# Performance work log

Measured on AMD Instinct MI355X. Metric: run time of the kernel, lower is better.

Reference implementation:

```python
import jax, jax.numpy as jnp
import numpy as np

N_NODES = 50000
N_EDGES = 400000
EMB_DIM = 256
N_LAYERS = 5
MAX_NODES = 50          # nodes per graph (equal-size graphs)
N_GRAPHS = N_NODES // MAX_NODES
BN_EPS = 1e-5


def setup_inputs() -> dict:
    key = jax.random.key(0)
    ks = jax.random.split(key, 12)
    D = EMB_DIM
    x = jax.random.normal(ks[0], (N_NODES, D), dtype=jnp.float32)
    edge_index = jax.random.randint(ks[1], (2, N_EDGES), 0, N_NODES, dtype=jnp.int64)
    edge_attr = jax.random.randint(ks[2], (N_EDGES, 2), 0, 3, dtype=jnp.int64)
    batch = (jnp.arange(N_NODES, dtype=jnp.int64) // MAX_NODES)
    # per-layer parameters, stacked on leading layer axis
    s1 = 1.0 / np.sqrt(D)
    s2 = 1.0 / np.sqrt(2 * D)
    W1 = jax.random.uniform(ks[3], (N_LAYERS, D, 2 * D), jnp.float32, -s1, s1)
    b1 = jax.random.uniform(ks[4], (N_LAYERS, 2 * D), jnp.float32, -s1, s1)
    W2 = jax.random.uniform(ks[5], (N_LAYERS, 2 * D, D), jnp.float32, -s2, s2)
    b2 = jax.random.uniform(ks[6], (N_LAYERS, D), jnp.float32, -s2, s2)
    # xavier_uniform for edge embeddings
    g1 = np.sqrt(6.0 / (6 + D))
    g2 = np.sqrt(6.0 / (3 + D))
    E1 = jax.random.uniform(ks[7], (N_LAYERS, 6, D), jnp.float32, -g1, g1)
    E2 = jax.random.uniform(ks[8], (N_LAYERS, 3, D), jnp.float32, -g2, g2)
    gamma = jnp.ones((N_LAYERS, D), jnp.float32)
    beta = jnp.zeros((N_LAYERS, D), jnp.float32)
    return {"x": x, "edge_index": edge_index, "edge_attr": edge_attr,
            "batch": batch, "W1": W1, "b1": b1, "W2": W2, "b2": b2,
            "E1": E1, "E2": E2, "gamma": gamma, "beta": beta}


def reference(x, edge_index, edge_attr, batch, W1, b1, W2, b2, E1, E2, gamma, beta):
    N, D = x.shape
    # add self loops once (edge_index/edge_attr are identical every layer);
    # self-loop edge_attr fill_value = 0
    loop = jnp.arange(N, dtype=edge_index.dtype)
    src = jnp.concatenate([edge_index[0], loop])
    dst = jnp.concatenate([edge_index[1], loop])
    ea0 = jnp.concatenate([edge_attr[:, 0], jnp.zeros((N,), edge_attr.dtype)])
    ea1 = jnp.concatenate([edge_attr[:, 1], jnp.zeros((N,), edge_attr.dtype)])

    h = x
    L = W1.shape[0]
    for l in range(L):
        # GINConv: message = x_j + edge_embedding, aggr='add', update = MLP
        eemb = E1[l][ea0] + E2[l][ea1]                       # [E+N, D]
        msg = h[src] + eemb                                   # gather + add
        agg = jax.ops.segment_sum(msg, dst, num_segments=N)   # scatter-add
        h = jnp.maximum(agg @ W1[l] + b1[l], 0.0) @ W2[l] + b2[l]
        # BatchNorm1d (training mode: batch statistics over nodes)
        mu = h.mean(axis=0)
        var = h.var(axis=0)
        h = (h - mu) / jnp.sqrt(var + BN_EPS) * gamma[l] + beta[l]
        if l < L - 1:
            h = jnp.maximum(h, 0.0)  # relu (dropout p=0 is identity)

    # pad_sequence over graphs: scatter node reps into [G, MAX_NODES, D]
    G = N // MAX_NODES
    ones = jnp.ones((N,), jnp.int32)
    counts = jax.ops.segment_sum(ones, batch, num_segments=G)
    starts = jnp.cumsum(counts) - counts
    pos = jnp.arange(N) - starts[batch]
    padded = jnp.zeros((G, MAX_NODES, D), h.dtype).at[batch, pos].set(h)
    return padded
```

## Files before the change

kernel.cpp:

```cpp
#include <hip/hip_runtime.h>

#define NN 50000
#define NE 400000
#define DIM 256
#define HID 512
#define NL 5
#define BN_EPS 1e-5f
#define NB_SCAN 196

typedef float float4v __attribute__((ext_vector_type(4)));
typedef _Float16 half8 __attribute__((ext_vector_type(8)));
typedef _Float16 half4v __attribute__((ext_vector_type(4)));

__device__ __forceinline__ void gl_lds16(const void* g, void* l) {
    __builtin_amdgcn_global_load_lds((__attribute__((address_space(1))) void*)g,
                                     (__attribute__((address_space(3))) void*)l, 16, 0, 0);
}


__global__ void k_zero(int* p, int n) {
    int i = blockIdx.x * blockDim.x + threadIdx.x;
    if (i < n) p[i] = 0;
}

__global__ void k_x2h(const float* __restrict__ x, _Float16* __restrict__ xh) {
    int i = blockIdx.x * blockDim.x + threadIdx.x;
    if (i >= NN * DIM / 4) return;
    float4 v = ((const float4*)x)[i];
    half4v o;
    o.x = (_Float16)v.x; o.y = (_Float16)v.y; o.z = (_Float16)v.z; o.w = (_Float16)v.w;
    ((half4v*)xh)[i] = o;
}

__global__ void k_ctab(const float* __restrict__ E1, const float* __restrict__ E2,
                       float* __restrict__ C) {
    int b = blockIdx.x;
    int l = b / 9, ab = b % 9;
    int a = ab / 3, bb = ab % 3;
    int c = threadIdx.x;
    C[(size_t)b * DIM + c] = E1[(size_t)(l * 6 + a) * DIM + c] + E2[(size_t)(l * 3 + bb) * DIM + c];
}

__global__ void k_hist(const int* __restrict__ ei, int* __restrict__ counts) {
    int e = blockIdx.x * blockDim.x + threadIdx.x;
    if (e < NE) atomicAdd(&counts[ei[NE + e]], 1);
}

__global__ void k_bsum(const int* __restrict__ counts, int* __restrict__ bsum) {
    __shared__ int s[256];
    int t = threadIdx.x;
    int i = blockIdx.x * 256 + t;
    s[t] = (i < NN) ? counts[i] : 0;
    __syncthreads();
    for (int off = 128; off > 0; off >>= 1) {
        if (t < off) s[t] += s[t + off];
        __syncthreads();
    }
    if (t == 0) bsum[blockIdx.x] = s[0];
}

__global__ void k_bscan(const int* __restrict__ bsum, int* __restrict__ bofs) {
    __shared__ int s[256];
    int t = threadIdx.x;
    int v = (t < NB_SCAN) ? bsum[t] : 0;
    s[t] = v;
    __syncthreads();
    for (int off = 1; off < 256; off <<= 1) {
        int u = (t >= off) ? s[t - off] : 0;
        __syncthreads();
        s[t] += u;
        __syncthreads();
    }
    if (t < NB_SCAN) bofs[t] = s[t] - v;
}

__global__ void k_scatterptr(const int* __restrict__ counts, const int* __restrict__ bofs,
                             int* __restrict__ row_ptr, int* __restrict__ cursor) {
    __shared__ int s[256];
    int t = threadIdx.x;
    int i = blockIdx.x * 256 + t;
    int v = (i < NN) ? counts[i] : 0;
    s[t] = v;
    __syncthreads();
    for (int off = 1; off < 256; off <<= 1) {
        int u = (t >= off) ? s[t - off] : 0;
        __syncthreads();
        s[t] += u;
        __syncthreads();
    }
    if (i < NN) {
        int ex = bofs[blockIdx.x] + s[t] - v;
        row_ptr[i] = ex;
        cursor[i] = ex;
    }
    if (i == NN - 1) row_ptr[NN] = NE;
}

__global__ void k_fill(const int* __restrict__ ei, const int* __restrict__ ea,
                       int* __restrict__ cursor, int* __restrict__ recs) {
    int e = blockIdx.x * blockDim.x + threadIdx.x;
    if (e >= NE) return;
    int src = ei[e];
    int dst = ei[NE + e];
    int a = ea[2 * e];
    int b = ea[2 * e + 1];
    int rec = src | ((a * 3 + b) << 20);
    int pos = atomicAdd(&cursor[dst], 1);
    recs[pos] = rec;
}

__global__ void k_wt(const float* __restrict__ W, _Float16* __restrict__ T, int K, int N) {
    __shared__ float t[32][33];
    int l = blockIdx.z;
    int k0 = blockIdx.y * 32, n0 = blockIdx.x * 32;
    int tx = threadIdx.x, ty = threadIdx.y;
    const float* Wl = W + (size_t)l * K * N;
    _Float16* Tl = T + (size_t)l * N * K;
    for (int d = 0; d < 32; d += 8)
        t[ty + d][tx] = Wl[(size_t)(k0 + ty + d) * N + n0 + tx];
    __syncthreads();
    for (int d = 0; d < 32; d += 8)
        Tl[(size_t)(n0 + ty + d) * K + k0 + tx] = (_Float16)t[tx][ty + d];
}

template <bool APPLY>
__global__ __launch_bounds__(256) void k_agg(const _Float16* __restrict__ rows,
                                             const float* __restrict__ ss,
                                             const float* __restrict__ Cl,
                                             const int* __restrict__ row_ptr,
                                             const int* __restrict__ recs,
                                             _Float16* __restrict__ aggh) {
    int node = (blockIdx.x * blockDim.x + threadIdx.x) >> 6;
    int lane = threadIdx.x & 63;
    if (node >= NN) return;
    int c = lane * 4;
    float s0 = 1.f, s1 = 1.f, s2 = 1.f, s3 = 1.f, t0 = 0.f, t1 = 0.f, t2 = 0.f, t3 = 0.f;
    if (APPLY) {
        s0 = ss[c]; s1 = ss[c + 1]; s2 = ss[c + 2]; s3 = ss[c + 3];
        t0 = ss[DIM + c]; t1 = ss[DIM + c + 1]; t2 = ss[DIM + c + 2]; t3 = ss[DIM + c + 3];
    }
    float4 cv0 = *(const float4*)(Cl + c);
    half4v sv = *(const half4v*)(rows + (size_t)node * DIM + c);
    float ax, ay, az, aw;
    if (APPLY) {
        ax = fmaxf((float)sv.x * s0 + t0, 0.f) + cv0.x;
        ay = fmaxf((float)sv.y * s1 + t1, 0.f) + cv0.y;
        az = fmaxf((float)sv.z * s2 + t2, 0.f) + cv0.z;
        aw = fmaxf((float)sv.w * s3 + t3, 0.f) + cv0.w;
    } else {
        ax = (float)sv.x + cv0.x;
        ay = (float)sv.y + cv0.y;
        az = (float)sv.z + cv0.z;
        aw = (float)sv.w + cv0.w;
    }
    int e0 = row_ptr[node], e1 = row_ptr[node + 1];
    for (int e = e0; e < e1; ++e) {
        int rec = recs[e];
        int src = rec & 0xFFFFF;
        int attr = rec >> 20;
        half4v hv = *(const half4v*)(rows + (size_t)src * DIM + c);
        float4 cv = *(const float4*)(Cl + (size_t)attr * DIM + c);
        if (APPLY) {
            ax += fmaxf((float)hv.x * s0 + t0, 0.f) + cv.x;
            ay += fmaxf((float)hv.y * s1 + t1, 0.f) + cv.y;
            az += fmaxf((float)hv.z * s2 + t2, 0.f) + cv.z;
            aw += fmaxf((float)hv.w * s3 + t3, 0.f) + cv.w;
        } else {
            ax += (float)hv.x + cv.x;
            ay += (float)hv.y + cv.y;
            az += (float)hv.z + cv.z;
            aw += (float)hv.w + cv.w;
        }
    }
    half4v o;
    o.x = (_Float16)ax; o.y = (_Float16)ay; o.z = (_Float16)az; o.w = (_Float16)aw;
    *(half4v*)(aggh + (size_t)node * DIM + c) = o;
}

__global__ __launch_bounds__(256, 2) void k_mlp(const _Float16* __restrict__ A,
                                                const _Float16* __restrict__ W1t,
                                                const float* __restrict__ b1,
                                                const _Float16* __restrict__ W2t,
                                                const float* __restrict__ b2,
                                                _Float16* __restrict__ Z,
                                                float* __restrict__ stats, int M) {
    __shared__ _Float16 ldsA[64 * 128];
    __shared__ _Float16 ldsH[64 * 512];
    int tid = threadIdx.x;
    int w = tid >> 6, lane = tid & 63;
    int lm = lane & 15, lg = lane >> 4;
    int row0 = blockIdx.x * 64;

    float4v acc1[4][8];
    const float4v zero = {0.f, 0.f, 0.f, 0.f};
#pragma unroll
    for (int i = 0; i < 4; ++i)
#pragma unroll
        for (int j = 0; j < 8; ++j) acc1[i][j] = zero;

#pragma unroll
    for (int kc = 0; kc < 2; ++kc) {
        {
            int srow = lane >> 4;
            int slot = lane & 15;
#pragma unroll
            for (int j = 0; j < 4; ++j) {
                int cr = w * 16 + j * 4 + srow;
                int gr = min(row0 + cr, M - 1);
                int gk = kc * 128 + ((slot ^ (cr & 7)) * 8);
                gl_lds16(A + (size_t)gr * DIM + gk, ldsA + (w * 16 + j * 4) * 128);
            }
        }
        __syncthreads();
#pragma unroll
        for (int qq = 0; qq < 4; ++qq) {
            half8 bf[8];
#pragma unroll
            for (int nt = 0; nt < 8; ++nt) {
                int n = w * 128 + nt * 16 + lm;
                bf[nt] = *(const half8*)(W1t + (size_t)n * DIM + kc * 128 + qq * 32 + lg * 8);
            }
            half8 af[4];
#pragma unroll
            for (int mt = 0; mt < 4; ++mt) {
                int m = mt * 16 + lm;
                int slot = qq * 4 + lg;
                af[mt] = *(const half8*)(ldsA + m * 128 + ((slot ^ (m & 7)) * 8));
            }
#pragma unroll
            for (int mt = 0; mt < 4; ++mt)
#pragma unroll
                for (int nt = 0; nt < 8; ++nt)
                    acc1[mt][nt] = __builtin_amdgcn_mfma_f32_16x16x32_f16(af[mt], bf[nt],
                                                                          acc1[mt][nt], 0, 0, 0);
        }
        __syncthreads();
    }

#pragma unroll
    for (int nt = 0; nt < 8; ++nt) {
        int col = w * 128 + nt * 16 + lm;
        float bv = b1[col];
        int cs = col >> 3, ci = col & 7;
#pragma unroll
        for (int mt = 0; mt < 4; ++mt)
#pragma unroll
            for (int r = 0; r < 4; ++r) {
                int row = mt * 16 + lg * 4 + r;
                float v = fmaxf(acc1[mt][nt][r] + bv, 0.f);
                ldsH[row * 512 + ((cs ^ (row & 7)) << 3) + ci] = (_Float16)v;
            }
    }
    __syncthreads();

    float4v acc2[4][4];
#pragma unroll
    for (int i = 0; i < 4; ++i)
#pragma unroll
        for (int j = 0; j < 4; ++j) acc2[i][j] = zero;

#pragma unroll
    for (int q = 0; q < 16; ++q) {
        half8 bf[4];
#pragma unroll
        for (int nt = 0; nt < 4; ++nt) {
            int n = w * 64 + nt * 16 + lm;
            bf[nt] = *(const half8*)(W2t + (size_t)n * HID + q * 32 + lg * 8);
        }
        half8 af[4];
#pragma unroll
        for (int mt = 0; mt < 4; ++mt) {
            int m = mt * 16 + lm;
            int slot = q * 4 + lg;
            af[mt] = *(const half8*)(ldsH + m * 512 + ((slot ^ (m & 7)) << 3));
        }
#pragma unroll
        for (int mt = 0; mt < 4; ++mt)
#pragma unroll
            for (int nt = 0; nt < 4; ++nt)
                acc2[mt][nt] = __builtin_amdgcn_mfma_f32_16x16x32_f16(af[mt], bf[nt],
                                                                      acc2[mt][nt], 0, 0, 0);
    }
    __syncthreads();

    _Float16* ldsZ = ldsH;
    float psum[4], psq[4];
#pragma unroll
    for (int nt = 0; nt < 4; ++nt) { psum[nt] = 0.f; psq[nt] = 0.f; }
#pragma unroll
    for (int nt = 0; nt < 4; ++nt) {
        int col = w * 64 + nt * 16 + lm;
        float bv = b2[col];
        int cs = col >> 3, ci = col & 7;
#pragma unroll
        for (int mt = 0; mt < 4; ++mt)
#pragma unroll
            for (int r = 0; r < 4; ++r) {
                int row = mt * 16 + lg * 4 + r;
                float v = acc2[mt][nt][r] + bv;
                if (row0 + row < M) {
                    psum[nt] += v;
                    psq[nt] += v * v;
                }
                ldsZ[row * 256 + ((cs ^ (row & 7)) << 3) + ci] = (_Float16)v;
            }
    }
#pragma unroll
    for (int nt = 0; nt < 4; ++nt) {
        psum[nt] += __shfl_xor(psum[nt], 16);
        psum[nt] += __shfl_xor(psum[nt], 32);
        psq[nt] += __shfl_xor(psq[nt], 16);
        psq[nt] += __shfl_xor(psq[nt], 32);
    }
    if (lg == 0) {
#pragma unroll
        for (int nt = 0; nt < 4; ++nt) {
            int ch = w * 64 + nt * 16 + lm;
            atomicAdd(&stats[ch], psum[nt]);
            atomicAdd(&stats[DIM + ch], psq[nt]);
        }
    }
    __syncthreads();
#pragma unroll
    for (int i = 0; i < 8; ++i) {
        int s = i * 256 + tid;
        int row = s >> 5, c16 = s & 31;
        if (row0 + row < M) {
            half8 v = *(const half8*)(ldsZ + row * 256 + ((c16 ^ (row & 7)) << 3));
            *(half8*)(Z + (size_t)(row0 + row) * DIM + c16 * 8) = v;
        }
    }
}

__global__ void k_bnfin(float* __restrict__ stats, const float* __restrict__ gamma,
                        const float* __restrict__ beta, float* __restrict__ ss) {
    int c = threadIdx.x;
    float mu = stats[c] * (1.0f / NN);
    float var = stats[DIM + c] * (1.0f / NN) - mu * mu;
    float sc = gamma[c] / sqrtf(var + BN_EPS);
    ss[c] = sc;
    ss[DIM + c] = beta[c] - mu * sc;
    stats[c] = 0.f;
    stats[DIM + c] = 0.f;
}

__global__ void k_out(const _Float16* __restrict__ z, const float* __restrict__ ss,
                      float* __restrict__ out) {
    int i = blockIdx.x * blockDim.x + threadIdx.x;
    if (i >= NN * DIM / 4) return;
    int c4 = (i & (DIM / 4 - 1)) * 4;
    half4v v = ((const half4v*)z)[i];
    float4 o;
    o.x = (float)v.x * ss[c4] + ss[DIM + c4];
    o.y = (float)v.y * ss[c4 + 1] + ss[DIM + c4 + 1];
    o.z = (float)v.z * ss[c4 + 2] + ss[DIM + c4 + 2];
    o.w = (float)v.w * ss[c4 + 3] + ss[DIM + c4 + 3];
    ((float4*)out)[i] = o;
}

extern "C" void kernel_launch(void* const* d_in, const int* in_sizes, int n_in,
                              void* d_out, int out_size, void* d_ws, size_t ws_size,
                              hipStream_t stream) {
    const float* x = (const float*)d_in[0];
    const int* ei = (const int*)d_in[1];
    const int* ea = (const int*)d_in[2];
    const float* W1 = (const float*)d_in[4];
    const float* b1 = (const float*)d_in[5];
    const float* W2 = (const float*)d_in[6];
    const float* b2 = (const float*)d_in[7];
    const float* E1 = (const float*)d_in[8];
    const float* E2 = (const float*)d_in[9];
    const float* gamma = (const float*)d_in[10];
    const float* beta = (const float*)d_in[11];
    float* out = (float*)d_out;

    char* w = (char*)d_ws;
    _Float16* xh = (_Float16*)w;   w += (size_t)NN * DIM * 2;
    _Float16* z = (_Float16*)w;    w += (size_t)NN * DIM * 2;
    _Float16* aggh = (_Float16*)w; w += (size_t)NN * DIM * 2;
    _Float16* W1t = (_Float16*)w;  w += (size_t)NL * DIM * HID * 2;
    _Float16* W2t = (_Float16*)w;  w += (size_t)NL * HID * DIM * 2;
    float* Ctab = (float*)w;       w += (size_t)NL * 9 * DIM * 4;
    float* stats = (float*)w;      w += 2 * DIM * 4;
    float* ss = (float*)w;         w += 2 * DIM * 4;
    int* row_ptr = (int*)w;        w += (size_t)(NN + 2) * 4;
    int* counts = (int*)w;         w += (size_t)NN * 4;
    int* cursor = (int*)w;         w += (size_t)NN * 4;
    int* bsum = (int*)w;           w += 256 * 4;
    int* bofs = (int*)w;           w += 256 * 4;
    int* recs = (int*)w;           w += (size_t)NE * 4;

    k_zero<<<(NN + 255) / 256, 256, 0, stream>>>(counts, NN);
    k_zero<<<2, 256, 0, stream>>>((int*)stats, 2 * DIM);
    k_x2h<<<(NN * DIM / 4 + 255) / 256, 256, 0, stream>>>(x, xh);
    k_ctab<<<NL * 9, 256, 0, stream>>>(E1, E2, Ctab);
    k_hist<<<(NE + 255) / 256, 256, 0, stream>>>(ei, counts);
    k_bsum<<<NB_SCAN, 256, 0, stream>>>(counts, bsum);
    k_bscan<<<1, 256, 0, stream>>>(bsum, bofs);
    k_scatterptr<<<NB_SCAN, 256, 0, stream>>>(counts, bofs, row_ptr, cursor);
    k_fill<<<(NE + 255) / 256, 256, 0, stream>>>(ei, ea, cursor, recs);
    {
        dim3 b(32, 8);
        dim3 g1(HID / 32, DIM / 32, NL);
        k_wt<<<g1, b, 0, stream>>>(W1, W1t, DIM, HID);
        dim3 g2(DIM / 32, HID / 32, NL);
        k_wt<<<g2, b, 0, stream>>>(W2, W2t, HID, DIM);
    }

    for (int l = 0; l < NL; ++l) {
        const float* Cl = Ctab + (size_t)l * 9 * DIM;
        if (l == 0)
            k_agg<false><<<(NN + 3) / 4, 256, 0, stream>>>(xh, ss, Cl, row_ptr, recs, aggh);
        else
            k_agg<true><<<(NN + 3) / 4, 256, 0, stream>>>(z, ss, Cl, row_ptr, recs, aggh);

        k_mlp<<<(NN + 63) / 64, 256, 0, stream>>>(aggh, W1t + (size_t)l * DIM * HID,
                                                  b1 + (size_t)l * HID,
                                                  W2t + (size_t)l * HID * DIM,
                                                  b2 + (size_t)l * DIM, z, stats, NN);

        k_bnfin<<<1, 256, 0, stream>>>(stats, gamma + (size_t)l * DIM, beta + (size_t)l * DIM, ss);
    }
    k_out<<<(NN * DIM / 4 + 255) / 256, 256, 0, stream>>>(z, ss, out);
}
```

Measured before the change: 875.9 us.

## Precount edge-attr combos per node, unroll gather, chunk hidden layer in MLP

Edge-embedding contributions are now folded algebraically: per-destination counts of each of the 9 attribute combos are built once during CSR fill, and each node adds count-weighted table rows instead of loading an embedding row per edge. The gather loop becomes a plain source-only loop unrolled by four for more memory-level parallelism. The fused MLP kernel is restructured to process the 512-wide hidden layer in four 128-column chunks, shrinking LDS and registers to allow 3 blocks per CU instead of 2. The cost is an extra atomic counter array per node and more synchronisation points inside the MLP.

```diff
diff --git a/kernel.cpp b/kernel.cpp
--- a/kernel.cpp
+++ b/kernel.cpp
@@ -97,16 +97,17 @@
 }
 
 __global__ void k_fill(const int* __restrict__ ei, const int* __restrict__ ea,
-                       int* __restrict__ cursor, int* __restrict__ recs) {
+                       int* __restrict__ cursor, int* __restrict__ srcs,
+                       int* __restrict__ cnt9) {
     int e = blockIdx.x * blockDim.x + threadIdx.x;
     if (e >= NE) return;
     int src = ei[e];
     int dst = ei[NE + e];
     int a = ea[2 * e];
     int b = ea[2 * e + 1];
-    int rec = src | ((a * 3 + b) << 20);
     int pos = atomicAdd(&cursor[dst], 1);
-    recs[pos] = rec;
+    srcs[pos] = src;
+    atomicAdd(&cnt9[dst * 9 + a * 3 + b], 1);
 }
 
 __global__ void k_wt(const float* __restrict__ W, _Float16* __restrict__ T, int K, int N) {
@@ -128,7 +129,8 @@
                                              const float* __restrict__ ss,
                                              const float* __restrict__ Cl,
                                              const int* __restrict__ row_ptr,
-                                             const int* __restrict__ recs,
+                                             const int* __restrict__ srcs,
+                                             const int* __restrict__ cnt9,
                                              _Float16* __restrict__ aggh) {
     int node = (blockIdx.x * blockDim.x + threadIdx.x) >> 6;
     int lane = threadIdx.x & 63;
@@ -139,151 +141,159 @@
         s0 = ss[c]; s1 = ss[c + 1]; s2 = ss[c + 2]; s3 = ss[c + 3];
         t0 = ss[DIM + c]; t1 = ss[DIM + c + 1]; t2 = ss[DIM + c + 2]; t3 = ss[DIM + c + 3];
     }
-    float4 cv0 = *(const float4*)(Cl + c);
-    half4v sv = *(const half4v*)(rows + (size_t)node * DIM + c);
-    float ax, ay, az, aw;
-    if (APPLY) {
-        ax = fmaxf((float)sv.x * s0 + t0, 0.f) + cv0.x;
-        ay = fmaxf((float)sv.y * s1 + t1, 0.f) + cv0.y;
-        az = fmaxf((float)sv.z * s2 + t2, 0.f) + cv0.z;
-        aw = fmaxf((float)sv.w * s3 + t3, 0.f) + cv0.w;
-    } else {
-        ax = (float)sv.x + cv0.x;
-        ay = (float)sv.y + cv0.y;
-        az = (float)sv.z + cv0.z;
-        aw = (float)sv.w + cv0.w;
+    float ax = 0.f, ay = 0.f, az = 0.f, aw = 0.f;
+#define ACC(hv)                                                   \
+    do {                                                          \
+        if (APPLY) {                                              \
+            ax += fmaxf((float)(hv).x * s0 + t0, 0.f);            \
+            ay += fmaxf((float)(hv).y * s1 + t1, 0.f);            \
+            az += fmaxf((float)(hv).z * s2 + t2, 0.f);            \
+            aw += fmaxf((float)(hv).w * s3 + t3, 0.f);            \
+        } else {                                                  \
+            ax += (float)(hv).x; ay += (float)(hv).y;             \
+            az += (float)(hv).z; aw += (float)(hv).w;             \
+        }                                                         \
+    } while (0)
+
+    {
+        half4v sv = *(const half4v*)(rows + (size_t)node * DIM + c);
+        ACC(sv);
     }
     int e0 = row_ptr[node], e1 = row_ptr[node + 1];
-    for (int e = e0; e < e1; ++e) {
-        int rec = recs[e];
-        int src = rec & 0xFFFFF;
-        int attr = rec >> 20;
-        half4v hv = *(const half4v*)(rows + (size_t)src * DIM + c);
-        float4 cv = *(const float4*)(Cl + (size_t)attr * DIM + c);
-        if (APPLY) {
-            ax += fmaxf((float)hv.x * s0 + t0, 0.f) + cv.x;
-            ay += fmaxf((float)hv.y * s1 + t1, 0.f) + cv.y;
-            az += fmaxf((float)hv.z * s2 + t2, 0.f) + cv.z;
-            aw += fmaxf((float)hv.w * s3 + t3, 0.f) + cv.w;
-        } else {
-            ax += (float)hv.x + cv.x;
-            ay += (float)hv.y + cv.y;
-            az += (float)hv.z + cv.z;
-            aw += (float)hv.w + cv.w;
-        }
+    int e = e0;
+    for (; e + 4 <= e1; e += 4) {
+        int i0 = srcs[e], i1 = srcs[e + 1], i2 = srcs[e + 2], i3 = srcs[e + 3];
+        half4v h0 = *(const half4v*)(rows + (size_t)i0 * DIM + c);
+        half4v h1 = *(const half4v*)(rows + (size_t)i1 * DIM + c);
+        half4v h2 = *(const half4v*)(rows + (size_t)i2 * DIM + c);
+        half4v h3 = *(const half4v*)(rows + (size_t)i3 * DIM + c);
+        ACC(h0); ACC(h1); ACC(h2); ACC(h3);
+    }
+    for (; e < e1; ++e) {
+        int i0 = srcs[e];
+        half4v h0 = *(const half4v*)(rows + (size_t)i0 * DIM + c);
+        ACC(h0);
+    }
+#undef ACC
+    const int* cn = cnt9 + (size_t)node * 9;
+#pragma unroll
+    for (int a = 0; a < 9; ++a) {
+        float f = (float)(cn[a] + (a == 0 ? 1 : 0));
+        float4 cv = *(const float4*)(Cl + (size_t)a * DIM + c);
+        ax += f * cv.x;
+        ay += f * cv.y;
+        az += f * cv.z;
+        aw += f * cv.w;
     }
     half4v o;
     o.x = (_Float16)ax; o.y = (_Float16)ay; o.z = (_Float16)az; o.w = (_Float16)aw;
     *(half4v*)(aggh + (size_t)node * DIM + c) = o;
 }
 
-__global__ __launch_bounds__(256, 2) void k_mlp(const _Float16* __restrict__ A,
+__global__ __launch_bounds__(256, 3) void k_mlp(const _Float16* __restrict__ A,
                                                 const _Float16* __restrict__ W1t,
                                                 const float* __restrict__ b1,
                                                 const _Float16* __restrict__ W2t,
                                                 const float* __restrict__ b2,
                                                 _Float16* __restrict__ Z,
                                                 float* __restrict__ stats, int M) {
-    __shared__ _Float16 ldsA[64 * 128];
-    __shared__ _Float16 ldsH[64 * 512];
+    __shared__ _Float16 ldsA[64 * 256];
+    __shared__ _Float16 ldsH[64 * 128];
     int tid = threadIdx.x;
     int w = tid >> 6, lane = tid & 63;
     int lm = lane & 15, lg = lane >> 4;
     int row0 = blockIdx.x * 64;
 
-    float4v acc1[4][8];
+    {
+        int srow = lane >> 5;
+        int slot = lane & 31;
+#pragma unroll
+        for (int j = 0; j < 8; ++j) {
+            int cr = w * 16 + j * 2 + srow;
+            int gr = min(row0 + cr, M - 1);
+            int gk = (slot ^ (cr & 7)) * 8;
+            gl_lds16(A + (size_t)gr * DIM + gk, ldsA + (w * 16 + j * 2) * 256);
+        }
+    }
+    __syncthreads();
+
+    float4v acc2[4][4];
     const float4v zero = {0.f, 0.f, 0.f, 0.f};
 #pragma unroll
     for (int i = 0; i < 4; ++i)
 #pragma unroll
-        for (int j = 0; j < 8; ++j) acc1[i][j] = zero;
-
-#pragma unroll
-    for (int kc = 0; kc < 2; ++kc) {
-        {
-            int srow = lane >> 4;
-            int slot = lane & 15;
-#pragma unroll
-            for (int j = 0; j < 4; ++j) {
-                int cr = w * 16 + j * 4 + srow;
-                int gr = min(row0 + cr, M - 1);
-                int gk = kc * 128 + ((slot ^ (cr & 7)) * 8);
-                gl_lds16(A + (size_t)gr * DIM + gk, ldsA + (w * 16 + j * 4) * 128);
-            }
-        }
-        __syncthreads();
-#pragma unroll
-        for (int qq = 0; qq < 4; ++qq) {
-            half8 bf[8];
-#pragma unroll
-            for (int nt = 0; nt < 8; ++nt) {
-                int n = w * 128 + nt * 16 + lm;
-                bf[nt] = *(const half8*)(W1t + (size_t)n * DIM + kc * 128 + qq * 32 + lg * 8);
+        for (int j = 0; j < 4; ++j) acc2[i][j] = zero;
+
+#pragma unroll
+    for (int ch = 0; ch < 4; ++ch) {
+        float4v acc1[4][2];
+#pragma unroll
+        for (int i = 0; i < 4; ++i)
+#pragma unroll
+            for (int j = 0; j < 2; ++j) acc1[i][j] = zero;
+#pragma unroll
+        for (int kq = 0; kq < 8; ++kq) {
+            half8 bf[2];
+#pragma unroll
+            for (int nt = 0; nt < 2; ++nt) {
+                int n = ch * 128 + w * 32 + nt * 16 + lm;
+                bf[nt] = *(const half8*)(W1t + (size_t)n * DIM + kq * 32 + lg * 8);
             }
             half8 af[4];
 #pragma unroll
             for (int mt = 0; mt < 4; ++mt) {
                 int m = mt * 16 + lm;
-                int slot = qq * 4 + lg;
-                af[mt] = *(const half8*)(ldsA + m * 128 + ((slot ^ (m & 7)) * 8));
+                int slot = kq * 4 + lg;
+                af[mt] = *(const half8*)(ldsA + m * 256 + ((slot ^ (m & 7)) * 8));
             }
 #pragma unroll
             for (int mt = 0; mt < 4; ++mt)
 #pragma unroll
-                for (int nt = 0; nt < 8; ++nt)
+                for (int nt = 0; nt < 2; ++nt)
                     acc1[mt][nt] = __builtin_amdgcn_mfma_f32_16x16x32_f16(af[mt], bf[nt],
                                                                           acc1[mt][nt], 0, 0, 0);
         }
-        __syncthreads();
-    }
-
-#pragma unroll
-    for (int nt = 0; nt < 8; ++nt) {
-        int col = w * 128 + nt * 16 + lm;
-        float bv = b1[col];
-        int cs = col >> 3, ci = col & 7;
-#pragma unroll
-        for (int mt = 0; mt < 4; ++mt)
-#pragma unroll
-            for (int r = 0; r < 4; ++r) {
-                int row = mt * 16 + lg * 4 + r;
-                float v = fmaxf(acc1[mt][nt][r] + bv, 0.f);
-                ldsH[row * 512 + ((cs ^ (row & 7)) << 3) + ci] = (_Float16)v;
+#pragma unroll
+        for (int nt = 0; nt < 2; ++nt) {
+            int hc = w * 32 + nt * 16 + lm;
+            float bv = b1[ch * 128 + hc];
+            int cs = hc >> 3, ci = hc & 7;
+#pragma unroll
+            for (int mt = 0; mt < 4; ++mt)
+#pragma unroll
+                for (int r = 0; r < 4; ++r) {
+                    int row = mt * 16 + lg * 4 + r;
+                    float v = fmaxf(acc1[mt][nt][r] + bv, 0.f);
+                    ldsH[row * 128 + ((cs ^ (row & 7)) << 3) + ci] = (_Float16)v;
+                }
+        }
+        __syncthreads();
+#pragma unroll
+        for (int kq = 0; kq < 4; ++kq) {
+            half8 bf[4];
+#pragma unroll
+            for (int nt = 0; nt < 4; ++nt) {
+                int n = w * 64 + nt * 16 + lm;
+                bf[nt] = *(const half8*)(W2t + (size_t)n * HID + ch * 128 + kq * 32 + lg * 8);
             }
-    }
-    __syncthreads();
-
-    float4v acc2[4][4];
-#pragma unroll
-    for (int i = 0; i < 4; ++i)
-#pragma unroll
-        for (int j = 0; j < 4; ++j) acc2[i][j] = zero;
-
-#pragma unroll
-    for (int q = 0; q < 16; ++q) {
-        half8 bf[4];
-#pragma unroll
-        for (int nt = 0; nt < 4; ++nt) {
-            int n = w * 64 + nt * 16 + lm;
-            bf[nt] = *(const half8*)(W2t + (size_t)n * HID + q * 32 + lg * 8);
-        }
-        half8 af[4];
-#pragma unroll
-        for (int mt = 0; mt < 4; ++mt) {
-            int m = mt * 16 + lm;
-            int slot = q * 4 + lg;
-            af[mt] = *(const half8*)(ldsH + m * 512 + ((slot ^ (m & 7)) << 3));
-        }
-#pragma unroll
-        for (int mt = 0; mt < 4; ++mt)
-#pragma unroll
-            for (int nt = 0; nt < 4; ++nt)
-                acc2[mt][nt] = __builtin_amdgcn_mfma_f32_16x16x32_f16(af[mt], bf[nt],
-                                                                      acc2[mt][nt], 0, 0, 0);
-    }
-    __syncthreads();
-
-    _Float16* ldsZ = ldsH;
+            half8 af[4];
+#pragma unroll
+            for (int mt = 0; mt < 4; ++mt) {
+                int m = mt * 16 + lm;
+                int slot = kq * 4 + lg;
+                af[mt] = *(const half8*)(ldsH + m * 128 + ((slot ^ (m & 7)) << 3));
+            }
+#pragma unroll
+            for (int mt = 0; mt < 4; ++mt)
+#pragma unroll
+                for (int nt = 0; nt < 4; ++nt)
+                    acc2[mt][nt] = __builtin_amdgcn_mfma_f32_16x16x32_f16(af[mt], bf[nt],
+                                                                          acc2[mt][nt], 0, 0, 0);
+        }
+        __syncthreads();
+    }
+
+    _Float16* ldsZ = ldsA;
     float psum[4], psq[4];
 #pragma unroll
     for (int nt = 0; nt < 4; ++nt) { psum[nt] = 0.f; psq[nt] = 0.f; }
@@ -315,9 +325,9 @@
     if (lg == 0) {
 #pragma unroll
         for (int nt = 0; nt < 4; ++nt) {
-            int ch = w * 64 + nt * 16 + lm;
-            atomicAdd(&stats[ch], psum[nt]);
-            atomicAdd(&stats[DIM + ch], psq[nt]);
+            int chn = w * 64 + nt * 16 + lm;
+            atomicAdd(&stats[chn], psum[nt]);
+            atomicAdd(&stats[DIM + chn], psq[nt]);
         }
     }
     __syncthreads();
@@ -388,9 +398,11 @@
     int* cursor = (int*)w;         w += (size_t)NN * 4;
     int* bsum = (int*)w;           w += 256 * 4;
     int* bofs = (int*)w;           w += 256 * 4;
-    int* recs = (int*)w;           w += (size_t)NE * 4;
+    int* srcs = (int*)w;           w += (size_t)NE * 4;
+    int* cnt9 = (int*)w;           w += (size_t)NN * 9 * 4;
 
     k_zero<<<(NN + 255) / 256, 256, 0, stream>>>(counts, NN);
+    k_zero<<<(NN * 9 + 255) / 256, 256, 0, stream>>>(cnt9, NN * 9);
     k_zero<<<2, 256, 0, stream>>>((int*)stats, 2 * DIM);
     k_x2h<<<(NN * DIM / 4 + 255) / 256, 256, 0, stream>>>(x, xh);
     k_ctab<<<NL * 9, 256, 0, stream>>>(E1, E2, Ctab);
@@ -398,7 +410,7 @@
     k_bsum<<<NB_SCAN, 256, 0, stream>>>(counts, bsum);
     k_bscan<<<1, 256, 0, stream>>>(bsum, bofs);
     k_scatterptr<<<NB_SCAN, 256, 0, stream>>>(counts, bofs, row_ptr, cursor);
-    k_fill<<<(NE + 255) / 256, 256, 0, stream>>>(ei, ea, cursor, recs);
+    k_fill<<<(NE + 255) / 256, 256, 0, stream>>>(ei, ea, cursor, srcs, cnt9);
     {
         dim3 b(32, 8);
         dim3 g1(HID / 32, DIM / 32, NL);
@@ -410,9 +422,9 @@
     for (int l = 0; l < NL; ++l) {
         const float* Cl = Ctab + (size_t)l * 9 * DIM;
         if (l == 0)
-            k_agg<false><<<(NN + 3) / 4, 256, 0, stream>>>(xh, ss, Cl, row_ptr, recs, aggh);
+            k_agg<false><<<(NN + 3) / 4, 256, 0, stream>>>(xh, ss, Cl, row_ptr, srcs, cnt9, aggh);
         else
-            k_agg<true><<<(NN + 3) / 4, 256, 0, stream>>>(z, ss, Cl, row_ptr, recs, aggh);
+            k_agg<true><<<(NN + 3) / 4, 256, 0, stream>>>(z, ss, Cl, row_ptr, srcs, cnt9, aggh);
 
         k_mlp<<<(NN + 63) / 64, 256, 0, stream>>>(aggh, W1t + (size_t)l * DIM * HID,
                                                   b1 + (size_t)l * HID,
```

Result: slower. 0.9999 ms (+14.2%).
